# Performance work log

Hardware: AMD Instinct MI355X
Metric: run time of the kernel (lower is better)

## Reference

```python
import jax, jax.numpy as jnp
import numpy as np

EPS = 1e-12  # F.normalize eps
NEG_SLOPE = 0.01  # F.leaky_relu default


def _neigh_agg(x, edge_index, W, b, num_node):
    # x: [N_src, d]; edge_index: [2, E]; W: [d, d]; b: [d]
    src, tgt = edge_index[0], edge_index[1]
    h = jax.nn.relu(x @ W + b)                      # [N_src, d]
    gathered = h[tgt]                               # [E, d] irregular gather
    aggr = jax.ops.segment_sum(gathered, src, num_segments=num_node)  # [N, d]
    deg = jax.ops.segment_sum(jnp.ones_like(src, dtype=aggr.dtype), src,
                              num_segments=num_node)
    deg = jnp.clip(deg, 1.0, None)
    return aggr / deg[:, None]                      # mean-aggregate; dropout is eval no-op


def setup_inputs() -> dict:
    key = jax.random.key(0)
    ks = jax.random.split(key, 16)
    N, E, d = 50000, 800000, 128
    f = lambda k, s: jax.random.normal(k, s, dtype=jnp.float32)
    inp = {
        "x_r": f(ks[0], (N, d)),
        "x_u": f(ks[1], (N, d)),
        "x_b": f(ks[2], (N, d)),
        "x_node": f(ks[3], (N, d)),
        "edges_r": jax.random.randint(ks[4], (2, E), 0, N),
        "edges_u": jax.random.randint(ks[5], (2, E), 0, N),
        "edges_b": jax.random.randint(ks[6], (2, E), 0, N),
        "num_node": N,
        # learned params (Linear weights stored as [in, out])
        "W_r": f(ks[7], (d, d)) * 0.05, "b_r": f(ks[8], (d,)) * 0.05,
        "W_u": f(ks[9], (d, d)) * 0.05, "b_u": f(ks[10], (d,)) * 0.05,
        "W_b": f(ks[11], (d, d)) * 0.05, "b_b": f(ks[12], (d,)) * 0.05,
        "u": f(ks[13], (2 * d, 1)),
        "W_lin": f(ks[14], (2 * d, d)) * 0.05, "b_lin": f(ks[15], (d,)) * 0.05,
    }
    return inp


def reference(x_r, x_u, x_b, x_node, edges_r, edges_u, edges_b, num_node,
              W_r, b_r, W_u, b_u, W_b, b_b, u, W_lin, b_lin):
    r_aggr = _neigh_agg(x_r, edges_r, W_r, b_r, num_node)  # [N, d]
    u_aggr = _neigh_agg(x_u, edges_u, W_u, b_u, num_node)
    b_aggr = _neigh_agg(x_b, edges_b, W_b, b_b, num_node)

    def score(aggr):
        cat = jnp.concatenate([aggr, x_node], axis=-1)      # [N, 2d]
        return jnp.exp(jax.nn.leaky_relu(cat @ u, NEG_SLOPE))  # [N, 1]

    r_s, u_s, b_s = score(r_aggr), score(u_aggr), score(b_aggr)
    denom = r_s + u_s + b_s
    combined = (r_s / denom) * r_aggr + (u_s / denom) * u_aggr + (b_s / denom) * b_aggr
    combined = jnp.concatenate([x_node, combined], axis=-1)  # [N, 2d]
    h = jax.nn.relu(combined @ W_lin + b_lin)                # [N, d]
    norm = jnp.maximum(jnp.linalg.norm(h, axis=-1, keepdims=True), EPS)
    return h / norm
```

## Files before the change

### kernel.cpp

```cpp
#include <hip/hip_runtime.h>

typedef unsigned int uint_t;

#define NPB 120
#define NBQ 420
#define CAP 16
#define TILE 4096
#define NFILL 192
#define CAPB 2432
#define RAWCAP CAPB
#define XSTR 132

__device__ __forceinline__ float bflo(unsigned int u) {
  union { unsigned int i; float f; } v; v.i = u << 16; return v.f;
}
__device__ __forceinline__ float bfhi(unsigned int u) {
  union { unsigned int i; float f; } v; v.i = u & 0xffff0000u; return v.f;
}
__device__ __forceinline__ unsigned short f2bf(float f) {
  union { float f; unsigned int i; } v; v.f = f;
  unsigned int u = v.i;
  return (unsigned short)((u + 0x7fffu + ((u >> 16) & 1u)) >> 16);
}
__device__ __forceinline__ unsigned int pack2bf(float a, float b) {
  return (unsigned int)f2bf(a) | ((unsigned int)f2bf(b) << 16);
}

__device__ __forceinline__ void gemm_role(
    const float* __restrict__ x, const float* __restrict__ W,
    const float* __restrict__ bb, unsigned short* __restrict__ hg,
    int N, int bx, float* xs) {
  int tid = threadIdx.x;
  long row0 = (long)bx * 32;
  const float4* xv = (const float4*)x;
  for (int idx = tid; idx < 1024; idx += 256) {
    int r = idx >> 5, k4 = idx & 31;
    long row = row0 + r;
    float4 v = (row < N) ? xv[row * 32 + k4] : make_float4(0.f, 0.f, 0.f, 0.f);
    *(float4*)&xs[r * XSTR + k4 * 4] = v;
  }
  __syncthreads();
  int w = tid >> 6, lane = tid & 63;
  int rg = lane >> 4;
  int c = w * 32 + (lane & 15) * 2;
  int wcol = c >> 1;
  float b0 = bb[c], b1 = bb[c + 1];
  float acc[8][2];
#pragma unroll
  for (int i = 0; i < 8; ++i) { acc[i][0] = b0; acc[i][1] = b1; }
  const float2* Wp = (const float2*)W;
  float2 wq[4];
#pragma unroll
  for (int kk = 0; kk < 4; ++kk) wq[kk] = Wp[kk * 64 + wcol];
  for (int k = 0; k < 128; k += 4) {
    float4 xr[8];
#pragma unroll
    for (int i = 0; i < 8; ++i) xr[i] = *(const float4*)&xs[(rg + 4 * i) * XSTR + k];
    float2 wn[4];
#pragma unroll
    for (int kk = 0; kk < 4; ++kk) wn[kk] = wq[kk];
    if (k + 4 < 128) {
#pragma unroll
      for (int kk = 0; kk < 4; ++kk) wn[kk] = Wp[(k + 4 + kk) * 64 + wcol];
    }
#pragma unroll
    for (int kk = 0; kk < 4; ++kk) {
#pragma unroll
      for (int i = 0; i < 8; ++i) {
        float xv_ = ((const float*)&xr[i])[kk];
        acc[i][0] += xv_ * wq[kk].x;
        acc[i][1] += xv_ * wq[kk].y;
      }
    }
#pragma unroll
    for (int kk = 0; kk < 4; ++kk) wq[kk] = wn[kk];
  }
#pragma unroll
  for (int i = 0; i < 8; ++i) {
    long row = row0 + rg + 4 * i;
    if (row < N) {
      float v0 = fmaxf(acc[i][0], 0.f), v1 = fmaxf(acc[i][1], 0.f);
      *(uint_t*)&hg[row * 128 + c] = pack2bf(v0, v1);
    }
  }
}

__global__ __launch_bounds__(256) void mega_kernel(
    const float* __restrict__ x0, const float* __restrict__ x1,
    const float* __restrict__ x2, const float* __restrict__ W0,
    const float* __restrict__ W1, const float* __restrict__ W2,
    const float* __restrict__ b0, const float* __restrict__ b1,
    const float* __restrict__ b2, const int* __restrict__ e0,
    const int* __restrict__ e1, const int* __restrict__ e2,
    int* __restrict__ ccnt, uint_t* __restrict__ gout,
    unsigned short* __restrict__ h, int N, int E, int nbG) {
  __shared__ __align__(16) char smem[CAP * NBQ * 4 + NBQ * 4];
  int bid = blockIdx.x;
  if (bid >= NFILL) {
    int idx = bid - NFILL;
    int g = idx / nbG;
    int bx = idx - g * nbG;
    const float* x  = (g == 0) ? x0 : (g == 1) ? x1 : x2;
    const float* W  = (g == 0) ? W0 : (g == 1) ? W1 : W2;
    const float* bb = (g == 0) ? b0 : (g == 1) ? b1 : b2;
    gemm_role(x, W, bb, h + (size_t)g * N * 128, N, bx, (float*)smem);
    return;
  }
  int g = bid >> 6, chunk = bid & 63;
  const int* edges = (g == 0) ? e0 : (g == 1) ? e1 : e2;
  int NB = (N + NPB - 1) / NPB;
  uint_t* stage = (uint_t*)smem;
  int* scnt = (int*)(smem + CAP * NBQ * 4);
  int* cnt = ccnt + (size_t)g * NB;
  uint_t* out = gout + (size_t)g * NB * CAPB;
  for (int i = threadIdx.x; i < NB; i += 256) scnt[i] = 0;
  __syncthreads();
  int per = (E + 63) >> 6;
  int beg = chunk * per;
  int end = beg + per; if (end > E) end = E;
  for (int t0 = beg; t0 < end; t0 += TILE) {
    int t1 = t0 + TILE; if (t1 > end) t1 = end;
    for (int e = t0 + threadIdx.x; e < t1; e += 256) {
      int src = edges[e], tgt = edges[E + e];
      int b = src / NPB;
      uint_t pair = ((uint_t)(src - b * NPB) << 16) | (uint_t)tgt;
      int idx = atomicAdd(&scnt[b], 1);
      if (idx < CAP) {
        stage[b * CAP + idx] = pair;
      } else {
        int s = atomicAdd(&cnt[b], 1);
        if (s < CAPB) out[(size_t)b * CAPB + s] = pair;
      }
    }
    __syncthreads();
    for (int b = threadIdx.x; b < NB; b += 256) {
      int c = scnt[b];
      if (c) {
        if (c > CAP) c = CAP;
        int base = atomicAdd(&cnt[b], c);
        for (int i = 0; i < c; ++i)
          if (base + i < CAPB) out[(size_t)b * CAPB + base + i] = stage[b * CAP + i];
        scnt[b] = 0;
      }
    }
    __syncthreads();
  }
}

__global__ __launch_bounds__(256) void agg_bucket_kernel(
    const int* __restrict__ ccnt, const uint_t* __restrict__ gout,
    const unsigned short* __restrict__ h, unsigned short* __restrict__ aggr,
    int N, int NB) {
  __shared__ uint_t raw[RAWCAP];
  __shared__ uint_t sorted[RAWCAP];
  __shared__ int hcnt[NPB];
  __shared__ int hoff[NPB + 1];
  __shared__ int hfill[NPB];
  int g = blockIdx.y, b = blockIdx.x;
  int tid = threadIdx.x, w = tid >> 6, lane = tid & 63;
  for (int i = tid; i < NPB; i += 256) hcnt[i] = 0;
  int cnt = ccnt[(size_t)g * NB + b];
  if (cnt > RAWCAP) cnt = RAWCAP;
  const uint_t* pr = gout + ((size_t)g * NB + b) * CAPB;
  for (int i = tid; i < cnt; i += 256) raw[i] = pr[i];
  __syncthreads();
  for (int i = tid; i < cnt; i += 256) atomicAdd(&hcnt[raw[i] >> 16], 1);
  __syncthreads();
  if (w == 0) {
    int i0 = lane * 2, i1 = lane * 2 + 1;
    int v0 = (i0 < NPB) ? hcnt[i0] : 0;
    int v1 = (i1 < NPB) ? hcnt[i1] : 0;
    int s = v0 + v1;
    int incl = s;
    for (int off = 1; off < 64; off <<= 1) {
      int t = __shfl_up(incl, off, 64);
      if (lane >= off) incl += t;
    }
    int excl = incl - s;
    if (i0 < NPB) { hoff[i0] = excl; hfill[i0] = excl; }
    if (i1 < NPB) { hoff[i1] = excl + v0; hfill[i1] = excl + v0; }
    if (lane == 63) hoff[NPB] = incl;
  }
  __syncthreads();
  for (int i = tid; i < cnt; i += 256) {
    uint_t p = raw[i];
    int slot = atomicAdd(&hfill[p >> 16], 1);
    sorted[slot] = p & 0xffffu;
  }
  __syncthreads();
  const uint_t* hb = (const uint_t*)(h + (size_t)g * N * 128) + lane;
  uint_t* ab = (uint_t*)(aggr + (size_t)g * N * 128);
  long nb0 = (long)b * NPB;
  for (int r = w; r < NPB; r += 4) {
    long node = nb0 + r;
    if (node >= N) break;
    int s = hoff[r], e = hoff[r + 1];
    int deg = e - s;
    float a0 = 0.f, a1 = 0.f;
    for (int j = 0; j < deg; j += 8) {
      uint_t off[8], v[8];
#pragma unroll
      for (int q = 0; q < 8; ++q) {
        int idx = j + q; if (idx >= deg) idx = deg - 1;
        off[q] = sorted[s + idx] << 6;
      }
#pragma unroll
      for (int q = 0; q < 8; ++q) v[q] = hb[off[q]];
      int m = deg - j; if (m > 8) m = 8;
#pragma unroll
      for (int q = 0; q < 8; ++q)
        if (q < m) { a0 += bflo(v[q]); a1 += bfhi(v[q]); }
    }
    float idg = 1.f / (float)(deg > 1 ? deg : 1);
    ab[node * 64 + lane] = pack2bf(a0 * idg, a1 * idg);
  }
}

#define CSTR 260
__global__ __launch_bounds__(256) void combine_final_kernel(
    const unsigned short* __restrict__ aggr, const float* __restrict__ x_node,
    const float* __restrict__ u, const float* __restrict__ W,
    const float* __restrict__ b, float* __restrict__ out, int N) {
  __shared__ float xs[32 * CSTR];
  __shared__ float rsum[4 * 32];
  int tid = threadIdx.x;
  long row0 = (long)blockIdx.x * 32;
  const float4* xv = (const float4*)x_node;
  for (int idx = tid; idx < 1024; idx += 256) {
    int r = idx >> 5, k4 = idx & 31;
    long row = row0 + r;
    float4 v = (row < N) ? xv[row * 32 + k4] : make_float4(0.f, 0.f, 0.f, 0.f);
    *(float4*)&xs[r * CSTR + k4 * 4] = v;
  }
  __syncthreads();

  int w = tid >> 6, lane = tid & 63;
  int r0 = w * 8;
  const uint_t* ap = (const uint_t*)aggr;
  float2 ua = ((const float2*)u)[lane];
  float2 ux = ((const float2*)u)[64 + lane];
#pragma unroll
  for (int i = 0; i < 8; ++i) {
    int r = r0 + i;
    long n = row0 + r;
    float c0 = 0.f, c1 = 0.f;
    if (n < N) {
      uint_t vr = ap[n * 64 + lane];
      uint_t vu = ap[((size_t)N + n) * 64 + lane];
      uint_t vb = ap[((size_t)2 * N + n) * 64 + lane];
      float ar0 = bflo(vr), ar1 = bfhi(vr);
      float au0 = bflo(vu), au1 = bfhi(vu);
      float ab0 = bflo(vb), ab1 = bfhi(vb);
      float2 xn = *(const float2*)&xs[r * CSTR + lane * 2];
      float pr = ua.x * ar0 + ua.y * ar1;
      float pu = ua.x * au0 + ua.y * au1;
      float pb = ua.x * ab0 + ua.y * ab1;
      float px = ux.x * xn.x + ux.y * xn.y;
      for (int m = 32; m >= 1; m >>= 1) {
        pr += __shfl_xor(pr, m, 64);
        pu += __shfl_xor(pu, m, 64);
        pb += __shfl_xor(pb, m, 64);
        px += __shfl_xor(px, m, 64);
      }
      float zr = pr + px, zu = pu + px, zb = pb + px;
      zr = zr > 0.f ? zr : 0.01f * zr;
      zu = zu > 0.f ? zu : 0.01f * zu;
      zb = zb > 0.f ? zb : 0.01f * zb;
      float sr = expf(zr), su = expf(zu), sb = expf(zb);
      float inv = 1.f / (sr + su + sb);
      float wr = sr * inv, wu = su * inv, wb = sb * inv;
      c0 = wr * ar0 + wu * au0 + wb * ab0;
      c1 = wr * ar1 + wu * au1 + wb * ab1;
    }
    float2 cc; cc.x = c0; cc.y = c1;
    *(float2*)&xs[r * CSTR + 128 + lane * 2] = cc;
  }
  __syncthreads();

  int rg = lane >> 4;
  int c = w * 32 + (lane & 15) * 2;
  int wcol = c >> 1;
  float b0 = b[c], b1 = b[c + 1];
  float acc[8][2];
#pragma unroll
  for (int i = 0; i < 8; ++i) { acc[i][0] = b0; acc[i][1] = b1; }
  const float2* Wp = (const float2*)W;
  float2 wq[4];
#pragma unroll
  for (int kk = 0; kk < 4; ++kk) wq[kk] = Wp[kk * 64 + wcol];
  for (int k = 0; k < 256; k += 4) {
    float4 xr[8];
#pragma unroll
    for (int i = 0; i < 8; ++i) xr[i] = *(const float4*)&xs[(rg + 4 * i) * CSTR + k];
    float2 wn[4];
#pragma unroll
    for (int kk = 0; kk < 4; ++kk) wn[kk] = wq[kk];
    if (k + 4 < 256) {
#pragma unroll
      for (int kk = 0; kk < 4; ++kk) wn[kk] = Wp[(k + 4 + kk) * 64 + wcol];
    }
#pragma unroll
    for (int kk = 0; kk < 4; ++kk) {
#pragma unroll
      for (int i = 0; i < 8; ++i) {
        float xv_ = ((const float*)&xr[i])[kk];
        acc[i][0] += xv_ * wq[kk].x;
        acc[i][1] += xv_ * wq[kk].y;
      }
    }
#pragma unroll
    for (int kk = 0; kk < 4; ++kk) wq[kk] = wn[kk];
  }
#pragma unroll
  for (int i = 0; i < 8; ++i) {
    float v0 = fmaxf(acc[i][0], 0.f), v1 = fmaxf(acc[i][1], 0.f);
    acc[i][0] = v0; acc[i][1] = v1;
    float ss = v0 * v0 + v1 * v1;
    ss += __shfl_xor(ss, 1, 64);
    ss += __shfl_xor(ss, 2, 64);
    ss += __shfl_xor(ss, 4, 64);
    ss += __shfl_xor(ss, 8, 64);
    if ((lane & 15) == 0) rsum[w * 32 + rg + 4 * i] = ss;
  }
  __syncthreads();
#pragma unroll
  for (int i = 0; i < 8; ++i) {
    int r = rg + 4 * i;
    long row = row0 + r;
    if (row < N) {
      float tot = rsum[r] + rsum[32 + r] + rsum[64 + r] + rsum[96 + r];
      float inv = 1.f / fmaxf(sqrtf(tot), 1e-12f);
      float2 o; o.x = acc[i][0] * inv; o.y = acc[i][1] * inv;
      *(float2*)&out[row * 128 + c] = o;
    }
  }
}

extern "C" void kernel_launch(void* const* d_in, const int* in_sizes, int n_in,
                              void* d_out, int out_size, void* d_ws, size_t ws_size,
                              hipStream_t stream) {
  const float* x_r    = (const float*)d_in[0];
  const float* x_u    = (const float*)d_in[1];
  const float* x_b    = (const float*)d_in[2];
  const float* x_node = (const float*)d_in[3];
  const int* e_r = (const int*)d_in[4];
  const int* e_u = (const int*)d_in[5];
  const int* e_b = (const int*)d_in[6];
  const float* W_r   = (const float*)d_in[8];
  const float* b_r   = (const float*)d_in[9];
  const float* W_u   = (const float*)d_in[10];
  const float* b_u   = (const float*)d_in[11];
  const float* W_b   = (const float*)d_in[12];
  const float* b_b   = (const float*)d_in[13];
  const float* u     = (const float*)d_in[14];
  const float* W_lin = (const float*)d_in[15];
  const float* b_lin = (const float*)d_in[16];

  int N = in_sizes[0] / 128;
  int E = in_sizes[4] / 2;
  int NB = (N + NPB - 1) / NPB;

  unsigned short* aggr = (unsigned short*)d_ws;
  unsigned short* h = aggr + (size_t)3 * N * 128;
  uint_t* gout = (uint_t*)(h + (size_t)3 * N * 128);
  int* ccnt = (int*)(gout + (size_t)3 * NB * CAPB);

  hipMemsetAsync(ccnt, 0, (size_t)3 * NB * sizeof(int), stream);

  dim3 blk(256);
  int nbG = (N + 31) / 32;
  dim3 gMega(NFILL + 3 * nbG);
  dim3 gAgg(NB, 3);
  dim3 gFinal((N + 31) / 32);

  mega_kernel<<<gMega, blk, 0, stream>>>(x_r, x_u, x_b, W_r, W_u, W_b,
                                         b_r, b_u, b_b, e_r, e_u, e_b,
                                         ccnt, gout, h, N, E, nbG);
  agg_bucket_kernel<<<gAgg, blk, 0, stream>>>(ccnt, gout, h, aggr, N, NB);
  combine_final_kernel<<<gFinal, blk, 0, stream>>>(aggr, x_node, u, W_lin,
                                                   b_lin, (float*)d_out, N);
}
```

Baseline: 435.4 us.

## Stream GEMM x rows from global with wave-uniform rows; pad bucket staging stride

The GEMM role no longer stages a 32x128 x tile in shared memory. Each wave now owns 8 consecutive rows and reads them straight from global memory with wave-uniform addresses, which removes the barrier and the LDS round trip. Each lane covers two columns across the full 128 width, and the x and W loads for the next step are software-prefetched. The edge-bucketing staging array is padded to a stride of 17 to reduce LDS bank conflicts in the per-bucket flush loop. In exchange, every wave re-reads x rows from cache with broadcast loads instead of sharing one LDS tile.

```diff
diff --git a/kernel.cpp b/kernel.cpp
--- a/kernel.cpp
+++ b/kernel.cpp
@@ -5,11 +5,11 @@
 #define NPB 120
 #define NBQ 420
 #define CAP 16
+#define CAPS 17
 #define TILE 4096
 #define NFILL 192
 #define CAPB 2432
 #define RAWCAP CAPB
-#define XSTR 132
 
 __device__ __forceinline__ float bflo(unsigned int u) {
   union { unsigned int i; float f; } v; v.i = u << 16; return v.f;
@@ -29,55 +29,58 @@
 __device__ __forceinline__ void gemm_role(
     const float* __restrict__ x, const float* __restrict__ W,
     const float* __restrict__ bb, unsigned short* __restrict__ hg,
-    int N, int bx, float* xs) {
+    int N, int bx) {
   int tid = threadIdx.x;
-  long row0 = (long)bx * 32;
-  const float4* xv = (const float4*)x;
-  for (int idx = tid; idx < 1024; idx += 256) {
-    int r = idx >> 5, k4 = idx & 31;
-    long row = row0 + r;
-    float4 v = (row < N) ? xv[row * 32 + k4] : make_float4(0.f, 0.f, 0.f, 0.f);
-    *(float4*)&xs[r * XSTR + k4 * 4] = v;
-  }
-  __syncthreads();
   int w = tid >> 6, lane = tid & 63;
-  int rg = lane >> 4;
-  int c = w * 32 + (lane & 15) * 2;
-  int wcol = c >> 1;
+  long row0 = (long)bx * 32 + (long)w * 8;
+  int c = lane * 2;
   float b0 = bb[c], b1 = bb[c + 1];
   float acc[8][2];
 #pragma unroll
   for (int i = 0; i < 8; ++i) { acc[i][0] = b0; acc[i][1] = b1; }
+  const float* xr[8];
+#pragma unroll
+  for (int i = 0; i < 8; ++i) {
+    long r = row0 + i;
+    if (r > (long)N - 1) r = (long)N - 1;
+    int off = __builtin_amdgcn_readfirstlane((int)(r * 128));
+    xr[i] = x + off;
+  }
   const float2* Wp = (const float2*)W;
-  float2 wq[4];
-#pragma unroll
-  for (int kk = 0; kk < 4; ++kk) wq[kk] = Wp[kk * 64 + wcol];
+  float4 xq[8], xn[8];
+  float2 wq[4], wn[4];
+#pragma unroll
+  for (int i = 0; i < 8; ++i) xq[i] = *(const float4*)(xr[i]);
+#pragma unroll
+  for (int kk = 0; kk < 4; ++kk) wq[kk] = Wp[kk * 64 + lane];
   for (int k = 0; k < 128; k += 4) {
-    float4 xr[8];
-#pragma unroll
-    for (int i = 0; i < 8; ++i) xr[i] = *(const float4*)&xs[(rg + 4 * i) * XSTR + k];
-    float2 wn[4];
+#pragma unroll
+    for (int i = 0; i < 8; ++i) xn[i] = xq[i];
 #pragma unroll
     for (int kk = 0; kk < 4; ++kk) wn[kk] = wq[kk];
     if (k + 4 < 128) {
 #pragma unroll
-      for (int kk = 0; kk < 4; ++kk) wn[kk] = Wp[(k + 4 + kk) * 64 + wcol];
+      for (int i = 0; i < 8; ++i) xn[i] = *(const float4*)(xr[i] + k + 4);
+#pragma unroll
+      for (int kk = 0; kk < 4; ++kk) wn[kk] = Wp[(k + 4 + kk) * 64 + lane];
     }
 #pragma unroll
     for (int kk = 0; kk < 4; ++kk) {
 #pragma unroll
       for (int i = 0; i < 8; ++i) {
-        float xv_ = ((const float*)&xr[i])[kk];
+        float xv_ = ((const float*)&xq[i])[kk];
         acc[i][0] += xv_ * wq[kk].x;
         acc[i][1] += xv_ * wq[kk].y;
       }
     }
 #pragma unroll
+    for (int i = 0; i < 8; ++i) xq[i] = xn[i];
+#pragma unroll
     for (int kk = 0; kk < 4; ++kk) wq[kk] = wn[kk];
   }
 #pragma unroll
   for (int i = 0; i < 8; ++i) {
-    long row = row0 + rg + 4 * i;
+    long row = row0 + i;
     if (row < N) {
       float v0 = fmaxf(acc[i][0], 0.f), v1 = fmaxf(acc[i][1], 0.f);
       *(uint_t*)&hg[row * 128 + c] = pack2bf(v0, v1);
@@ -94,7 +97,8 @@
     const int* __restrict__ e1, const int* __restrict__ e2,
     int* __restrict__ ccnt, uint_t* __restrict__ gout,
     unsigned short* __restrict__ h, int N, int E, int nbG) {
-  __shared__ __align__(16) char smem[CAP * NBQ * 4 + NBQ * 4];
+  __shared__ uint_t stage[CAPS * NBQ];
+  __shared__ int scnt[NBQ];
   int bid = blockIdx.x;
   if (bid >= NFILL) {
     int idx = bid - NFILL;
@@ -103,14 +107,12 @@
     const float* x  = (g == 0) ? x0 : (g == 1) ? x1 : x2;
     const float* W  = (g == 0) ? W0 : (g == 1) ? W1 : W2;
     const float* bb = (g == 0) ? b0 : (g == 1) ? b1 : b2;
-    gemm_role(x, W, bb, h + (size_t)g * N * 128, N, bx, (float*)smem);
+    gemm_role(x, W, bb, h + (size_t)g * N * 128, N, bx);
     return;
   }
   int g = bid >> 6, chunk = bid & 63;
   const int* edges = (g == 0) ? e0 : (g == 1) ? e1 : e2;
   int NB = (N + NPB - 1) / NPB;
-  uint_t* stage = (uint_t*)smem;
-  int* scnt = (int*)(smem + CAP * NBQ * 4);
   int* cnt = ccnt + (size_t)g * NB;
   uint_t* out = gout + (size_t)g * NB * CAPB;
   for (int i = threadIdx.x; i < NB; i += 256) scnt[i] = 0;
@@ -126,7 +128,7 @@
       uint_t pair = ((uint_t)(src - b * NPB) << 16) | (uint_t)tgt;
       int idx = atomicAdd(&scnt[b], 1);
       if (idx < CAP) {
-        stage[b * CAP + idx] = pair;
+        stage[b * CAPS + idx] = pair;
       } else {
         int s = atomicAdd(&cnt[b], 1);
         if (s < CAPB) out[(size_t)b * CAPB + s] = pair;
@@ -139,7 +141,7 @@
         if (c > CAP) c = CAP;
         int base = atomicAdd(&cnt[b], c);
         for (int i = 0; i < c; ++i)
-          if (base + i < CAPB) out[(size_t)b * CAPB + base + i] = stage[b * CAP + i];
+          if (base + i < CAPB) out[(size_t)b * CAPB + base + i] = stage[b * CAPS + i];
         scnt[b] = 0;
       }
     }
```

New measurement: 492.8 us. 1.13x slower.
